# Performance work log

Measured on AMD Instinct MI355X. Metric: run time of the kernel, lower is better.

Reference implementation:

```python
import jax, jax.numpy as jnp
import numpy as np

NUM_LABELS_I = 28  # 7 entity types * 4 (B/I/E/S)
NUM_LABELS = 31    # + O, EOS, BOS
INDEX_O, INDEX_EOS, INDEX_BOS = 28, 29, 30
NEG = -10000.0


def _make_trans(rng):
    # replicate ChainCRF4NestedNER.reset_parameters() structural masking
    bs = np.arange(0, NUM_LABELS_I, 4)
    is_ = bs + 1
    es = bs + 2
    ss = bs + 3
    t = (rng.standard_normal((NUM_LABELS, NUM_LABELS)) * 0.1).astype(np.float32)
    for i in bs:
        t[i, :i + 1] = NEG; t[i, i + 3:] = NEG
    for i in is_:
        t[i, :i] = NEG; t[i, i + 2:] = NEG
    for i in np.concatenate([es, ss, [INDEX_O]]):
        t[i, is_] = NEG; t[i, es] = NEG; t[i, INDEX_BOS] = NEG
    t[INDEX_EOS, :INDEX_EOS] = NEG; t[INDEX_EOS, INDEX_BOS] = NEG
    t[INDEX_BOS, is_] = NEG; t[INDEX_BOS, es] = NEG; t[INDEX_BOS, INDEX_BOS] = NEG
    return jnp.asarray(t)


def setup_inputs() -> dict:
    B, T, D = 64, 512, 768
    key = jax.random.key(0)
    k1, k2, k3 = jax.random.split(key, 3)
    inp = jax.random.normal(k1, (B, T, D), dtype=jnp.float32)
    target = jax.random.randint(k2, (B, T), 0, 29, dtype=jnp.int64)  # real labels + O only
    mask = jnp.ones((B, T), dtype=jnp.float32)
    state_w = jax.random.normal(k3, (NUM_LABELS, D), dtype=jnp.float32) * 0.02
    state_b = jnp.concatenate([jnp.zeros(INDEX_EOS, jnp.float32),
                               jnp.full(NUM_LABELS - INDEX_EOS, NEG, jnp.float32)])
    trans = _make_trans(np.random.default_rng(0))
    return {"input": inp, "target": target, "mask": mask,
            "state_w": state_w, "state_b": state_b, "trans": trans}


def reference(input, target, mask, state_w, state_b, trans):
    B, T, _ = input.shape
    # state scores [B, T, L]
    out_s = jnp.einsum('btd,ld->btl', input, state_w) + state_b
    out_s = out_s.at[:, :, INDEX_EOS].add((mask == 0).astype(out_s.dtype) * 20000.0)
    # energy [B, T, L, L]: trans[prev, curr] + state[curr]
    energy = trans[None, None, :, :] + out_s[:, :, None, :]
    # forward algorithm (logsumexp semiring) as a scan over time
    energy_t = jnp.moveaxis(energy, 1, 0)  # [T, B, L, L]
    part0 = energy_t[0, :, INDEX_BOS, :]   # [B, L]

    def step(part, e_t):
        new = jax.nn.logsumexp(e_t + part[:, :, None], axis=1)
        return new, None

    partition, _ = jax.lax.scan(step, part0, energy_t[1:])
    # gold-path energy: sum_t energy[b, t, prev_label, label]
    prev = jnp.concatenate([jnp.full((B, 1), INDEX_BOS, dtype=target.dtype),
                            target[:, :-1]], axis=1)
    bi = jnp.arange(B)[:, None]
    ti = jnp.arange(T)[None, :]
    tgt_energy = energy[bi, ti, prev, target].sum(axis=1)
    loss = jax.nn.logsumexp(trans[:, INDEX_EOS][None, :] + partition, axis=1) - tgt_energy
    return loss, energy
```

## Files before the change

kernel.cpp:

```cpp
#include <hip/hip_runtime.h>

typedef float f32x4  __attribute__((ext_vector_type(4)));
typedef float f32x16 __attribute__((ext_vector_type(16)));
typedef short s16x8  __attribute__((ext_vector_type(8)));

constexpr int NL  = 31;
constexpr int BB  = 64;
constexpr int TT  = 512;
constexpr int DD  = 768;
constexpr int RTOT = BB * TT;
constexpr int IDX_EOS = 29;
constexpr int IDX_BOS = 30;
constexpr float LOG2E = 1.4426950408889634f;
constexpr float LN2F  = 0.6931471805599453f;

union Frag8 { unsigned u[4]; s16x8 s; };

__device__ inline unsigned pk2(float a, float b) {
  unsigned ua = __float_as_uint(a), ub = __float_as_uint(b);
  ua = (ua + 0x7fffu + ((ua >> 16) & 1u)) >> 16;
  ub = (ub + 0x7fffu + ((ub >> 16) & 1u)) >> 16;
  return ua | (ub << 16);
}
__device__ inline unsigned short bf16r(float a) {
  unsigned ua = __float_as_uint(a);
  return (unsigned short)((ua + 0x7fffu + ((ua >> 16) & 1u)) >> 16);
}

__device__ inline float bfly_max32(float v) {
#define STEPM(K) { float o = __int_as_float(__builtin_amdgcn_ds_swizzle(__float_as_int(v), ((K) << 10) | 0x1f)); v = fmaxf(v, o); }
  STEPM(1) STEPM(2) STEPM(4) STEPM(8) STEPM(16)
#undef STEPM
  return v;
}
__device__ inline float bfly_sum32(float v) {
#define STEPS(K) { float o = __int_as_float(__builtin_amdgcn_ds_swizzle(__float_as_int(v), ((K) << 10) | 0x1f)); v = v + o; }
  STEPS(1) STEPS(2) STEPS(4) STEPS(8) STEPS(16)
#undef STEPS
  return v;
}

__device__ inline void repack(const float E[16], int h, Frag8& B1, Frag8& B2) {
  unsigned o1a = pk2(E[4 * h], E[4 * h + 1]), o1b = pk2(E[4 * h + 2], E[4 * h + 3]);
  unsigned o2a = pk2(E[8 + 4 * h], E[8 + 4 * h + 1]), o2b = pk2(E[8 + 4 * h + 2], E[8 + 4 * h + 3]);
  int hb = 4 * (1 - h);
  unsigned s1a = pk2(E[hb], E[hb + 1]),         s1b = pk2(E[hb + 2], E[hb + 3]);
  unsigned s2a = pk2(E[8 + hb], E[8 + hb + 1]), s2b = pk2(E[8 + hb + 2], E[8 + hb + 3]);
  unsigned r1a = __shfl_xor((int)s1a, 32), r1b = __shfl_xor((int)s1b, 32);
  unsigned r2a = __shfl_xor((int)s2a, 32), r2b = __shfl_xor((int)s2b, 32);
  if (h == 0) {
    B1.u[0] = o1a; B1.u[1] = o1b; B1.u[2] = r1a; B1.u[3] = r1b;
    B2.u[0] = o2a; B2.u[1] = o2b; B2.u[2] = r2a; B2.u[3] = r2b;
  } else {
    B1.u[0] = r1a; B1.u[1] = r1b; B1.u[2] = o1a; B1.u[3] = o1b;
    B2.u[0] = r2a; B2.u[1] = r2b; B2.u[2] = o2a; B2.u[3] = o2b;
  }
}

__device__ inline void renorm16(float E[16], float& Sacc) {
  float m = E[0];
#pragma unroll
  for (int r = 1; r < 16; ++r) m = fmaxf(m, E[r]);
  m = bfly_max32(m);
  m = fmaxf(m, __shfl_xor(m, 32));
  float lg = truncf(log2f(m));
  Sacc += lg;
  float sc = exp2f(-lg);
#pragma unroll
  for (int r = 0; r < 16; ++r) E[r] *= sc;
}

__device__ inline void load_A16(const unsigned short* M, int l, int h, Frag8& A1, Frag8& A2) {
  A1.s = *(const s16x8*)(M + l * 32 + 8 * h);
  A2.s = *(const s16x8*)(M + l * 32 + 16 + 8 * h);
}
__device__ inline void load_B16(const unsigned short* M, int l, int h, Frag8& B1, Frag8& B2) {
#pragma unroll
  for (int m = 0; m < 4; ++m) {
    int k = 8 * h + 2 * m;
    unsigned lo0 = M[k * 32 + l],        hi0 = M[(k + 1) * 32 + l];
    unsigned lo1 = M[(k + 16) * 32 + l], hi1 = M[(k + 17) * 32 + l];
    B1.u[m] = lo0 | (hi0 << 16);
    B2.u[m] = lo1 | (hi1 << 16);
  }
}

__device__ inline void tree_node(unsigned short* Tb, float* Ts, int ja, int jb, int l, int h) {
  Frag8 A1, A2, B1, B2;
  load_A16(Tb + ja * 1024, l, h, A1, A2);
  load_B16(Tb + jb * 1024, l, h, B1, B2);
  f32x16 D = {};
  D = __builtin_amdgcn_mfma_f32_32x32x16_bf16(A1.s, B1.s, D, 0, 0, 0);
  D = __builtin_amdgcn_mfma_f32_32x32x16_bf16(A2.s, B2.s, D, 0, 0, 0);
  float E[16];
#pragma unroll
  for (int r = 0; r < 16; ++r) E[r] = D[r];
  float S = Ts[ja] + Ts[jb];
  renorm16(E, S);
#pragma unroll
  for (int r = 0; r < 16; ++r) {
    int row = (r & 3) + 8 * (r >> 2) + 4 * h;
    Tb[jb * 1024 + row * 32 + l] = bf16r(E[r]);
  }
  if (l == 0 && h == 0) Ts[jb] = S;
}

__device__ inline void energy_rows(float* dst0, const float* tr_p, const float* osh,
                                   int rbeg, int rend, int lane) {
  for (int r = rbeg; r < rend; ++r) {
    float* drow = dst0 + (size_t)r * 961;
    const float* orow = osh + r * 64;
#pragma unroll
    for (int it = 0; it < 4; ++it) {
      int e = it * 256 + lane * 4;
      if (e <= 957) {
        f32x4 t4 = *(const f32x4*)(tr_p + e);
        unsigned j = (unsigned)e - 31u * (((unsigned)e * 67651u) >> 21);
        f32x4 val;
#pragma unroll
        for (int k = 0; k < 4; ++k) val[k] = t4[k] + orow[j + k];
        *(f32x4*)(drow + e) = val;
      } else if (e == 960) {
        drow[960] = tr_p[960] + orow[30];
      }
    }
  }
}

__global__ void k_prep(const float* __restrict__ sw, unsigned short* __restrict__ Bw) {
  for (int i = blockIdx.x * 256 + threadIdx.x; i < 32 * DD; i += 8 * 256)
    Bw[i] = (i < NL * DD) ? bf16r(sw[i]) : (unsigned short)0;
}

__global__ __launch_bounds__(256, 8) void k_fused(
    const float* __restrict__ inp, const unsigned short* __restrict__ Bw,
    const float* __restrict__ sb, const float* __restrict__ msk,
    const float* __restrict__ trans, const int* __restrict__ target,
    float* __restrict__ energy, float* __restrict__ ws_partial,
    unsigned short* __restrict__ Mb, float* __restrict__ Sb,
    float* __restrict__ out0)
{
  __shared__ __align__(16) union {
    float accbuf[4][16][33];
    unsigned short Ms[4][1024];
  } ovl;
  __shared__ __align__(16) float tr_p[964];
  __shared__ __align__(16) float osh[16 * 64];
  __shared__ __align__(16) float ubw[4][128];
  __shared__ float Ss[4];

  int tid = threadIdx.x, wave = tid >> 6, lane = tid & 63;
  int bid = blockIdx.x;
  int r0 = bid * 16;
  int quad = lane >> 4, l15 = lane & 15;

  {
    int kcb = 3 * wave;
    const float* arow = inp + (size_t)(r0 + l15) * DD + kcb * 64 + quad * 8;
    f32x4 pa0a = *(const f32x4*)(arow);
    f32x4 pa0b = *(const f32x4*)(arow + 4);
    f32x4 pa1a = *(const f32x4*)(arow + 32);
    f32x4 pa1b = *(const f32x4*)(arow + 36);

    f32x4 acc[2] = {};
#pragma unroll
    for (int kc = 0; kc < 3; ++kc) {
      Frag8 af0, af1;
      af0.u[0] = pk2(pa0a[0], pa0a[1]); af0.u[1] = pk2(pa0a[2], pa0a[3]);
      af0.u[2] = pk2(pa0b[0], pa0b[1]); af0.u[3] = pk2(pa0b[2], pa0b[3]);
      af1.u[0] = pk2(pa1a[0], pa1a[1]); af1.u[1] = pk2(pa1a[2], pa1a[3]);
      af1.u[2] = pk2(pa1b[0], pa1b[1]); af1.u[3] = pk2(pa1b[2], pa1b[3]);
      if (kc < 2) {
        const float* a2 = arow + (kc + 1) * 64;
        pa0a = *(const f32x4*)(a2);      pa0b = *(const f32x4*)(a2 + 4);
        pa1a = *(const f32x4*)(a2 + 32); pa1b = *(const f32x4*)(a2 + 36);
      }
#pragma unroll
      for (int ct = 0; ct < 2; ++ct) {
        const unsigned short* bp = Bw + (ct * 16 + l15) * DD + (kcb + kc) * 64 + quad * 8;
        s16x8 bf0 = *(const s16x8*)(bp);
        acc[ct] = __builtin_amdgcn_mfma_f32_16x16x32_bf16(af0.s, bf0, acc[ct], 0, 0, 0);
        s16x8 bf1 = *(const s16x8*)(bp + 32);
        acc[ct] = __builtin_amdgcn_mfma_f32_16x16x32_bf16(af1.s, bf1, acc[ct], 0, 0, 0);
      }
    }
#pragma unroll
    for (int ct = 0; ct < 2; ++ct)
#pragma unroll
      for (int r = 0; r < 4; ++r)
        ovl.accbuf[wave][quad * 4 + r][ct * 16 + l15] = acc[ct][r];
  }
  __syncthreads();

  {
#pragma unroll
    for (int u = 0; u < 2; ++u) {
      int v = tid * 2 + u;
      int lr = v >> 5, col = v & 31;
      if (col < NL) {
        float s = ovl.accbuf[0][lr][col] + ovl.accbuf[1][lr][col]
                + ovl.accbuf[2][lr][col] + ovl.accbuf[3][lr][col];
        s += sb[col];
        if (col == IDX_EOS && msk[r0 + lr] == 0.f) s += 20000.f;
        osh[lr * 64 + col] = s;
        osh[lr * 64 + 31 + col] = s;
      }
    }
    for (int idx = tid; idx < 964; idx += 256) tr_p[idx] = (idx < 961) ? trans[idx] : 0.f;
  }
  __syncthreads();

  if ((bid & 31) == 0 && tid < NL) out0[(bid >> 5) * NL + tid] = osh[tid];

  int l = lane & 31, h = lane >> 5;

  {
    int s0 = ((bid & 31) == 0 && wave == 0) ? 1 : 0;
    float* ub = ubw[wave];
#pragma unroll
    for (int it = 0; it < 2; ++it) {
      int idx = lane + it * 64;
      int row = idx >> 5, col = idx & 31;
      float v = 0.f;
      if (col < NL) v = exp2f(LOG2E * osh[(4 * wave + row) * 64 + col]);
      ub[idx] = v;
    }

    Frag8 A1, A2, B1, B2;
#pragma unroll
    for (int m = 0; m < 4; ++m) {
      int k0 = 8 * h + 2 * m, k1 = k0 + 1;
      float a0 = (k0 < NL && l < NL) ? exp2f(LOG2E * tr_p[k0 * NL + l]) : 0.f;
      float a1 = (k1 < NL && l < NL) ? exp2f(LOG2E * tr_p[k1 * NL + l]) : 0.f;
      A1.u[m] = pk2(a0, a1);
      int k2 = 16 + k0, k3 = 16 + k1;
      float a2 = (k2 < NL && l < NL) ? exp2f(LOG2E * tr_p[k2 * NL + l]) : 0.f;
      float a3 = (k3 < NL && l < NL) ? exp2f(LOG2E * tr_p[k3 * NL + l]) : 0.f;
      A2.u[m] = pk2(a2, a3);
      B1.u[m] = ((k0 == l) ? 0x3f80u : 0u) | (((k1 == l) ? 0x3f80u : 0u) << 16);
      B2.u[m] = ((k2 == l) ? 0x3f80u : 0u) | (((k3 == l) ? 0x3f80u : 0u) << 16);
    }

    float E[16];
    for (int s = s0; s < 4; ++s) {
      const float* us = ub + s * 32 + 4 * h;
      f32x4 u0 = *(const f32x4*)(us);
      f32x4 u1 = *(const f32x4*)(us + 8);
      f32x4 u2 = *(const f32x4*)(us + 16);
      f32x4 u3 = *(const f32x4*)(us + 24);
      f32x16 D = {};
      D = __builtin_amdgcn_mfma_f32_32x32x16_bf16(A1.s, B1.s, D, 0, 0, 0);
      D = __builtin_amdgcn_mfma_f32_32x32x16_bf16(A2.s, B2.s, D, 0, 0, 0);
#pragma unroll
      for (int jj = 0; jj < 4; ++jj) {
        E[jj]      = D[jj]      * u0[jj];
        E[4 + jj]  = D[4 + jj]  * u1[jj];
        E[8 + jj]  = D[8 + jj]  * u2[jj];
        E[12 + jj] = D[12 + jj] * u3[jj];
      }
      if (s < 3) repack(E, h, B1, B2);
    }
    float S = 0.f;
    renorm16(E, S);
    unsigned short* mo = ovl.Ms[wave];
#pragma unroll
    for (int r = 0; r < 16; ++r) {
      int row = (r & 3) + 8 * (r >> 2) + 4 * h;
      mo[row * 32 + l] = bf16r(E[r]);
    }
    if (lane == 0) Ss[wave] = S;
  }
  __syncthreads();

  if (wave == 0) {
    Frag8 A1, A2, B1, B2;
    load_B16(ovl.Ms[0], l, h, B1, B2);
    float Sx = Ss[0] + Ss[1] + Ss[2] + Ss[3];
    float E2[16];
#pragma unroll
    for (int i = 1; i < 4; ++i) {
      load_A16(ovl.Ms[i], l, h, A1, A2);
      f32x16 D = {};
      D = __builtin_amdgcn_mfma_f32_32x32x16_bf16(A1.s, B1.s, D, 0, 0, 0);
      D = __builtin_amdgcn_mfma_f32_32x32x16_bf16(A2.s, B2.s, D, 0, 0, 0);
#pragma unroll
      for (int r = 0; r < 16; ++r) E2[r] = D[r];
      if (i < 3) repack(E2, h, B1, B2);
    }
    renorm16(E2, Sx);
    unsigned short* qo = Mb + (size_t)bid * 1024;
#pragma unroll
    for (int r = 0; r < 16; ++r) {
      int row = (r & 3) + 8 * (r >> 2) + 4 * h;
      qo[row * 32 + l] = bf16r(E2[r]);
    }
    if (lane == 0) Sb[bid] = Sx;

    energy_rows(energy + (size_t)r0 * 961, tr_p, osh, 15, 16, lane);
  } else {
    if (wave == 1 && lane < 16) {
      int r = r0 + lane;
      int tg = target[r];
      int prv = ((r & (TT - 1)) == 0) ? IDX_BOS : target[r - 1];
      float cc = tr_p[prv * NL + tg] + osh[lane * 64 + tg];
#pragma unroll
      for (int off = 8; off; off >>= 1) cc += __shfl_down(cc, off);
      if (lane == 0) ws_partial[bid] = cc;
    }
    int rb = 5 * (wave - 1);
    energy_rows(energy + (size_t)r0 * 961, tr_p, osh, rb, rb + 5, lane);
  }
}

__global__ __launch_bounds__(256) void k_tree(
    const float* __restrict__ trans, const unsigned short* __restrict__ Mb,
    const float* __restrict__ Sb, const float* __restrict__ ws_partial,
    const float* __restrict__ out0, float* __restrict__ loss)
{
  __shared__ __align__(16) unsigned short T[32][1024];
  __shared__ float Ts[32];
  __shared__ float wsh[32];
  int tid = threadIdx.x, wave = tid >> 6, lane = tid & 63;
  int l = lane & 31, h = lane >> 5;
  int b = blockIdx.x;

  const f32x4* src = (const f32x4*)(Mb + (size_t)b * 32 * 1024);
  f32x4* dstT = (f32x4*)T;
#pragma unroll
  for (int i = 0; i < 16; ++i) dstT[tid + i * 256] = src[tid + i * 256];
  if (tid < 32) {
    Ts[tid] = Sb[b * 32 + tid];
    wsh[tid] = ws_partial[b * 32 + tid];
  }
  __syncthreads();

  unsigned short* T0 = T[0];
#pragma unroll
  for (int i = 0; i < 4; ++i) { int j = wave + 4 * i; tree_node(T0, Ts, 2 * j + 1, 2 * j, l, h); }
  __syncthreads();
#pragma unroll
  for (int i = 0; i < 2; ++i) { int j = wave + 4 * i; tree_node(T0, Ts, 4 * j + 2, 4 * j, l, h); }
  __syncthreads();
  { int j = wave; tree_node(T0, Ts, 8 * j + 4, 8 * j, l, h); }
  __syncthreads();
  if (wave < 2) { int j = wave; tree_node(T0, Ts, 16 * j + 8, 16 * j, l, h); }
  __syncthreads();

  if (wave == 0) {
    Frag8 A1, A2, B1, B2;
    load_A16(T0 + 16 * 1024, l, h, A1, A2);
    load_B16(T0, l, h, B1, B2);
    f32x16 D = {};
    D = __builtin_amdgcn_mfma_f32_32x32x16_bf16(A1.s, B1.s, D, 0, 0, 0);
    D = __builtin_amdgcn_mfma_f32_32x32x16_bf16(A2.s, B2.s, D, 0, 0, 0);
    float E[16];
#pragma unroll
    for (int r = 0; r < 16; ++r) E[r] = D[r];
    float S = Ts[0] + Ts[16];

    float p0 = (l < NL) ? exp2f(LOG2E * (trans[IDX_BOS * NL + l] + out0[b * NL + l])) : 0.f;
    float sum_h = 0.f;
#pragma unroll
    for (int r = 0; r < 16; ++r) {
      float s = bfly_sum32(E[r] * p0);
      int row = (r & 3) + 8 * (r >> 2) + 4 * h;
      float We = (row < NL) ? exp2f(LOG2E * trans[row * NL + IDX_EOS]) : 0.f;
      sum_h += s * We;
    }
    float tot = sum_h + __shfl_xor(sum_h, 32);
    if (lane == 0) {
      float wst = 0.f;
#pragma unroll
      for (int i = 0; i < 32; ++i) wst += wsh[i];
      loss[b] = LN2F * (S + log2f(tot)) - wst;
    }
  }
}

extern "C" void kernel_launch(void* const* d_in, const int* in_sizes, int n_in,
                              void* d_out, int out_size, void* d_ws, size_t ws_size,
                              hipStream_t stream) {
  const float* inp   = (const float*)d_in[0];
  const int*   tgt   = (const int*)d_in[1];
  const float* msk   = (const float*)d_in[2];
  const float* sw    = (const float*)d_in[3];
  const float* sb    = (const float*)d_in[4];
  const float* trans = (const float*)d_in[5];

  float* out    = (float*)d_out;
  float* loss   = out;
  float* energy = out + BB;

  float* ws_partial = (float*)d_ws;
  float* Sb   = ws_partial + 2048;
  float* out0 = Sb + 2048;
  unsigned short* Mb = (unsigned short*)(out0 + 2048);
  unsigned short* Bw = Mb + (size_t)2048 * 1024;

  k_prep<<<8, 256, 0, stream>>>(sw, Bw);
  k_fused<<<RTOT / 16, 256, 0, stream>>>(inp, Bw, sb, msk, trans, tgt,
                                         energy, ws_partial, Mb, Sb, out0);
  k_tree<<<BB, 256, 0, stream>>>(trans, Mb, Sb, ws_partial, out0, loss);
}
```

Before: 294.5 us.

## Stage input tile via global_load_lds, align energy stores, skip tree renorms

The input rows are loaded straight into a swizzled LDS tile with global_load_lds instead of per-lane register loads. The tile is unioned with the other scratch arrays, and launch bounds drop to 3 blocks per SM to make room for it. Four shifted copies of trans let each energy row be written with 16-byte-aligned vector stores, with scalar head and tail stores. Renormalisation is skipped at three of the four tree levels in k_tree to save work. This risks bf16 overflow or underflow in the tree products and lowers occupancy.

```diff
diff --git a/kernel.cpp b/kernel.cpp
--- a/kernel.cpp
+++ b/kernel.cpp
@@ -25,6 +25,12 @@
 __device__ inline unsigned short bf16r(float a) {
   unsigned ua = __float_as_uint(a);
   return (unsigned short)((ua + 0x7fffu + ((ua >> 16) & 1u)) >> 16);
+}
+
+__device__ inline void gload16(const float* g, void* l) {
+  __builtin_amdgcn_global_load_lds(
+      (__attribute__((address_space(1))) void*)(void*)g,
+      (__attribute__((address_space(3))) void*)l, 16, 0, 0);
 }
 
 __device__ inline float bfly_max32(float v) {
@@ -85,6 +91,7 @@
   }
 }
 
+template<bool RN>
 __device__ inline void tree_node(unsigned short* Tb, float* Ts, int ja, int jb, int l, int h) {
   Frag8 A1, A2, B1, B2;
   load_A16(Tb + ja * 1024, l, h, A1, A2);
@@ -96,7 +103,7 @@
 #pragma unroll
   for (int r = 0; r < 16; ++r) E[r] = D[r];
   float S = Ts[ja] + Ts[jb];
-  renorm16(E, S);
+  if (RN) renorm16(E, S);
 #pragma unroll
   for (int r = 0; r < 16; ++r) {
     int row = (r & 3) + 8 * (r >> 2) + 4 * h;
@@ -105,23 +112,34 @@
   if (l == 0 && h == 0) Ts[jb] = S;
 }
 
-__device__ inline void energy_rows(float* dst0, const float* tr_p, const float* osh,
+__device__ inline void energy_rows(float* dst0, const float trs[4][964],
+                                   const float osh[16][34],
                                    int rbeg, int rend, int lane) {
   for (int r = rbeg; r < rend; ++r) {
+    int off = (4 - (r & 3)) & 3;
+    int S = (961 - off) >> 2;
+    const float* tcopy = trs[off];
+    const float* orow = osh[r];
     float* drow = dst0 + (size_t)r * 961;
-    const float* orow = osh + r * 64;
 #pragma unroll
     for (int it = 0; it < 4; ++it) {
-      int e = it * 256 + lane * 4;
-      if (e <= 957) {
-        f32x4 t4 = *(const f32x4*)(tr_p + e);
+      int slot = lane + (it << 6);
+      if (slot < S) {
+        int e = off + (slot << 2);
+        f32x4 t4 = *(const f32x4*)(tcopy + (slot << 2));
         unsigned j = (unsigned)e - 31u * (((unsigned)e * 67651u) >> 21);
         f32x4 val;
 #pragma unroll
         for (int k = 0; k < 4; ++k) val[k] = t4[k] + orow[j + k];
         *(f32x4*)(drow + e) = val;
-      } else if (e == 960) {
-        drow[960] = tr_p[960] + orow[30];
+      } else if (it == 3) {
+        int t = slot - S;
+        int total = 961 - (S << 2);
+        if (t < total) {
+          int e = (t < off) ? t : ((S << 2) + t);
+          unsigned j = (unsigned)e - 31u * (((unsigned)e * 67651u) >> 21);
+          drow[e] = trs[0][e] + orow[j];
+        }
       }
     }
   }
@@ -132,7 +150,7 @@
     Bw[i] = (i < NL * DD) ? bf16r(sw[i]) : (unsigned short)0;
 }
 
-__global__ __launch_bounds__(256, 8) void k_fused(
+__global__ __launch_bounds__(256, 3) void k_fused(
     const float* __restrict__ inp, const unsigned short* __restrict__ Bw,
     const float* __restrict__ sb, const float* __restrict__ msk,
     const float* __restrict__ trans, const int* __restrict__ target,
@@ -140,41 +158,55 @@
     unsigned short* __restrict__ Mb, float* __restrict__ Sb,
     float* __restrict__ out0)
 {
-  __shared__ __align__(16) union {
-    float accbuf[4][16][33];
-    unsigned short Ms[4][1024];
-  } ovl;
-  __shared__ __align__(16) float tr_p[964];
-  __shared__ __align__(16) float osh[16 * 64];
-  __shared__ __align__(16) float ubw[4][128];
-  __shared__ float Ss[4];
+  __shared__ __align__(1024) union SM {
+    float tileF[16][768];
+    struct {
+      float accbuf[4][16][33];
+      float trs[4][964];
+      float osh[16][34];
+      float ubw[4][128];
+      unsigned short Ms[4][1024];
+      float Ss[4];
+    } p;
+  } sm;
 
   int tid = threadIdx.x, wave = tid >> 6, lane = tid & 63;
   int bid = blockIdx.x;
   int r0 = bid * 16;
   int quad = lane >> 4, l15 = lane & 15;
+  int l = lane & 31, h = lane >> 5;
 
   {
+#pragma unroll
+    for (int rr = 0; rr < 4; ++rr) {
+      int r = wave * 4 + rr;
+      int s = r & 7;
+      const float* gr = inp + (size_t)(r0 + r) * DD;
+      float* lrow = &sm.tileF[r][0];
+#pragma unroll
+      for (int j = 0; j < 3; ++j)
+        gload16(gr + (j * 64 + (lane ^ s)) * 4, lrow + j * 256);
+    }
+  }
+  __syncthreads();
+
+  f32x4 acc[2] = {};
+  {
+    int sA = l15 & 7;
+    const float* tf = &sm.tileF[l15][0];
     int kcb = 3 * wave;
-    const float* arow = inp + (size_t)(r0 + l15) * DD + kcb * 64 + quad * 8;
-    f32x4 pa0a = *(const f32x4*)(arow);
-    f32x4 pa0b = *(const f32x4*)(arow + 4);
-    f32x4 pa1a = *(const f32x4*)(arow + 32);
-    f32x4 pa1b = *(const f32x4*)(arow + 36);
-
-    f32x4 acc[2] = {};
 #pragma unroll
     for (int kc = 0; kc < 3; ++kc) {
+      int u0 = (kcb + kc) * 16 + quad * 2;
+      f32x4 a0 = *(const f32x4*)(tf + ((u0)     ^ sA) * 4);
+      f32x4 a1 = *(const f32x4*)(tf + ((u0 + 1) ^ sA) * 4);
+      f32x4 a2 = *(const f32x4*)(tf + ((u0 + 8) ^ sA) * 4);
+      f32x4 a3 = *(const f32x4*)(tf + ((u0 + 9) ^ sA) * 4);
       Frag8 af0, af1;
-      af0.u[0] = pk2(pa0a[0], pa0a[1]); af0.u[1] = pk2(pa0a[2], pa0a[3]);
-      af0.u[2] = pk2(pa0b[0], pa0b[1]); af0.u[3] = pk2(pa0b[2], pa0b[3]);
-      af1.u[0] = pk2(pa1a[0], pa1a[1]); af1.u[1] = pk2(pa1a[2], pa1a[3]);
-      af1.u[2] = pk2(pa1b[0], pa1b[1]); af1.u[3] = pk2(pa1b[2], pa1b[3]);
-      if (kc < 2) {
-        const float* a2 = arow + (kc + 1) * 64;
-        pa0a = *(const f32x4*)(a2);      pa0b = *(const f32x4*)(a2 + 4);
-        pa1a = *(const f32x4*)(a2 + 32); pa1b = *(const f32x4*)(a2 + 36);
-      }
+      af0.u[0] = pk2(a0[0], a0[1]); af0.u[1] = pk2(a0[2], a0[3]);
+      af0.u[2] = pk2(a1[0], a1[1]); af0.u[3] = pk2(a1[2], a1[3]);
+      af1.u[0] = pk2(a2[0], a2[1]); af1.u[1] = pk2(a2[2], a2[3]);
+      af1.u[2] = pk2(a3[0], a3[1]); af1.u[3] = pk2(a3[2], a3[3]);
 #pragma unroll
       for (int ct = 0; ct < 2; ++ct) {
         const unsigned short* bp = Bw + (ct * 16 + l15) * DD + (kcb + kc) * 64 + quad * 8;
@@ -184,11 +216,19 @@
         acc[ct] = __builtin_amdgcn_mfma_f32_16x16x32_bf16(af1.s, bf1, acc[ct], 0, 0, 0);
       }
     }
+  }
+  __syncthreads();
+
+  {
 #pragma unroll
     for (int ct = 0; ct < 2; ++ct)
 #pragma unroll
       for (int r = 0; r < 4; ++r)
-        ovl.accbuf[wave][quad * 4 + r][ct * 16 + l15] = acc[ct][r];
+        sm.p.accbuf[wave][quad * 4 + r][ct * 16 + l15] = acc[ct][r];
+#pragma unroll
+    for (int s = 0; s < 4; ++s)
+      for (int i = tid; i < 964; i += 256)
+        sm.p.trs[s][i] = (i + s < 961) ? trans[i + s] : 0.f;
   }
   __syncthreads();
 
@@ -198,31 +238,28 @@
       int v = tid * 2 + u;
       int lr = v >> 5, col = v & 31;
       if (col < NL) {
-        float s = ovl.accbuf[0][lr][col] + ovl.accbuf[1][lr][col]
-                + ovl.accbuf[2][lr][col] + ovl.accbuf[3][lr][col];
+        float s = sm.p.accbuf[0][lr][col] + sm.p.accbuf[1][lr][col]
+                + sm.p.accbuf[2][lr][col] + sm.p.accbuf[3][lr][col];
         s += sb[col];
         if (col == IDX_EOS && msk[r0 + lr] == 0.f) s += 20000.f;
-        osh[lr * 64 + col] = s;
-        osh[lr * 64 + 31 + col] = s;
+        sm.p.osh[lr][col] = s;
+        if (col < 3) sm.p.osh[lr][31 + col] = s;
       }
     }
-    for (int idx = tid; idx < 964; idx += 256) tr_p[idx] = (idx < 961) ? trans[idx] : 0.f;
-  }
-  __syncthreads();
-
-  if ((bid & 31) == 0 && tid < NL) out0[(bid >> 5) * NL + tid] = osh[tid];
-
-  int l = lane & 31, h = lane >> 5;
+  }
+  __syncthreads();
+
+  if ((bid & 31) == 0 && tid < NL) out0[(bid >> 5) * NL + tid] = sm.p.osh[0][tid];
 
   {
     int s0 = ((bid & 31) == 0 && wave == 0) ? 1 : 0;
-    float* ub = ubw[wave];
+    float* ub = sm.p.ubw[wave];
 #pragma unroll
     for (int it = 0; it < 2; ++it) {
       int idx = lane + it * 64;
       int row = idx >> 5, col = idx & 31;
       float v = 0.f;
-      if (col < NL) v = exp2f(LOG2E * osh[(4 * wave + row) * 64 + col]);
+      if (col < NL) v = exp2f(LOG2E * sm.p.osh[4 * wave + row][col]);
       ub[idx] = v;
     }
 
@@ -230,12 +267,12 @@
 #pragma unroll
     for (int m = 0; m < 4; ++m) {
       int k0 = 8 * h + 2 * m, k1 = k0 + 1;
-      float a0 = (k0 < NL && l < NL) ? exp2f(LOG2E * tr_p[k0 * NL + l]) : 0.f;
-      float a1 = (k1 < NL && l < NL) ? exp2f(LOG2E * tr_p[k1 * NL + l]) : 0.f;
+      float a0 = (k0 < NL && l < NL) ? exp2f(LOG2E * sm.p.trs[0][k0 * NL + l]) : 0.f;
+      float a1 = (k1 < NL && l < NL) ? exp2f(LOG2E * sm.p.trs[0][k1 * NL + l]) : 0.f;
       A1.u[m] = pk2(a0, a1);
       int k2 = 16 + k0, k3 = 16 + k1;
-      float a2 = (k2 < NL && l < NL) ? exp2f(LOG2E * tr_p[k2 * NL + l]) : 0.f;
-      float a3 = (k3 < NL && l < NL) ? exp2f(LOG2E * tr_p[k3 * NL + l]) : 0.f;
+      float a2 = (k2 < NL && l < NL) ? exp2f(LOG2E * sm.p.trs[0][k2 * NL + l]) : 0.f;
+      float a3 = (k3 < NL && l < NL) ? exp2f(LOG2E * sm.p.trs[0][k3 * NL + l]) : 0.f;
       A2.u[m] = pk2(a2, a3);
       B1.u[m] = ((k0 == l) ? 0x3f80u : 0u) | (((k1 == l) ? 0x3f80u : 0u) << 16);
       B2.u[m] = ((k2 == l) ? 0x3f80u : 0u) | (((k3 == l) ? 0x3f80u : 0u) << 16);
@@ -262,24 +299,25 @@
     }
     float S = 0.f;
     renorm16(E, S);
-    unsigned short* mo = ovl.Ms[wave];
+    unsigned short* mo = sm.p.Ms[wave];
 #pragma unroll
     for (int r = 0; r < 16; ++r) {
       int row = (r & 3) + 8 * (r >> 2) + 4 * h;
       mo[row * 32 + l] = bf16r(E[r]);
     }
-    if (lane == 0) Ss[wave] = S;
-  }
-  __syncthreads();
-
+    if (lane == 0) sm.p.Ss[wave] = S;
+  }
+  __syncthreads();
+
+  float* dst0 = energy + (size_t)r0 * 961;
   if (wave == 0) {
     Frag8 A1, A2, B1, B2;
-    load_B16(ovl.Ms[0], l, h, B1, B2);
-    float Sx = Ss[0] + Ss[1] + Ss[2] + Ss[3];
+    load_B16(sm.p.Ms[0], l, h, B1, B2);
+    float Sx = sm.p.Ss[0] + sm.p.Ss[1] + sm.p.Ss[2] + sm.p.Ss[3];
     float E2[16];
 #pragma unroll
     for (int i = 1; i < 4; ++i) {
-      load_A16(ovl.Ms[i], l, h, A1, A2);
+      load_A16(sm.p.Ms[i], l, h, A1, A2);
       f32x16 D = {};
       D = __builtin_amdgcn_mfma_f32_32x32x16_bf16(A1.s, B1.s, D, 0, 0, 0);
       D = __builtin_amdgcn_mfma_f32_32x32x16_bf16(A2.s, B2.s, D, 0, 0, 0);
@@ -295,20 +333,19 @@
       qo[row * 32 + l] = bf16r(E2[r]);
     }
     if (lane == 0) Sb[bid] = Sx;
-
-    energy_rows(energy + (size_t)r0 * 961, tr_p, osh, 15, 16, lane);
+    energy_rows(dst0, sm.p.trs, sm.p.osh, 15, 16, lane);
   } else {
     if (wave == 1 && lane < 16) {
       int r = r0 + lane;
       int tg = target[r];
       int prv = ((r & (TT - 1)) == 0) ? IDX_BOS : target[r - 1];
-      float cc = tr_p[prv * NL + tg] + osh[lane * 64 + tg];
+      float cc = sm.p.trs[0][prv * NL + tg] + sm.p.osh[lane][tg];
 #pragma unroll
       for (int off = 8; off; off >>= 1) cc += __shfl_down(cc, off);
       if (lane == 0) ws_partial[bid] = cc;
     }
     int rb = 5 * (wave - 1);
-    energy_rows(energy + (size_t)r0 * 961, tr_p, osh, rb, rb + 5, lane);
+    energy_rows(dst0, sm.p.trs, sm.p.osh, rb, rb + 5, lane);
   }
 }
 
@@ -336,14 +373,14 @@
 
   unsigned short* T0 = T[0];
 #pragma unroll
-  for (int i = 0; i < 4; ++i) { int j = wave + 4 * i; tree_node(T0, Ts, 2 * j + 1, 2 * j, l, h); }
-  __syncthreads();
-#pragma unroll
-  for (int i = 0; i < 2; ++i) { int j = wave + 4 * i; tree_node(T0, Ts, 4 * j + 2, 4 * j, l, h); }
-  __syncthreads();
-  { int j = wave; tree_node(T0, Ts, 8 * j + 4, 8 * j, l, h); }
-  __syncthreads();
-  if (wave < 2) { int j = wave; tree_node(T0, Ts, 16 * j + 8, 16 * j, l, h); }
+  for (int i = 0; i < 4; ++i) { int j = wave + 4 * i; tree_node<false>(T0, Ts, 2 * j + 1, 2 * j, l, h); }
+  __syncthreads();
+#pragma unroll
+  for (int i = 0; i < 2; ++i) { int j = wave + 4 * i; tree_node<false>(T0, Ts, 4 * j + 2, 4 * j, l, h); }
+  __syncthreads();
+  { int j = wave; tree_node<true>(T0, Ts, 8 * j + 4, 8 * j, l, h); }
+  __syncthreads();
+  if (wave < 2) { int j = wave; tree_node<false>(T0, Ts, 16 * j + 8, 16 * j, l, h); }
   __syncthreads();
 
   if (wave == 0) {
```

New measurement: 269.1 us. -8.6%, faster.
